# Optimization experiments

Measured on AMD Instinct MI355X. Metric: run time of the kernel, lower is better.

## Reference

```python
import jax, jax.numpy as jnp
import numpy as np


def setup_inputs() -> dict:
    key = jax.random.key(0)
    ks = jax.random.split(key, 6)
    B, S, T, E, D = 16, 128, 128, 512, 512  # batch, enc steps, dec steps, enc units, dec units
    scale = 0.05
    return {
        "enc": jax.random.normal(ks[0], (B, S, E), dtype=jnp.float32),
        "dec": jax.random.normal(ks[1], (B, T, D), dtype=jnp.float32),
        "W1": jax.random.normal(ks[2], (E, E), dtype=jnp.float32) * scale,
        "W2": jax.random.normal(ks[3], (D, E), dtype=jnp.float32) * scale,
        "b": jax.random.normal(ks[4], (1, 1, E), dtype=jnp.float32) * scale,
        "V": jax.random.normal(ks[5], (E, 1), dtype=jnp.float32) * scale,
    }


def reference(enc, dec, W1, W2, b, V):
    # Vectorized Bahdanau additive attention (the original loops over decoder
    # timesteps with keras.backend.rnn; the steps are independent so we batch them).
    W1_hs = jnp.einsum('bse,ef->bsf', enc, W1)            # [B,S,E] (computed once, not per step)
    W2_ht = jnp.einsum('btd,de->bte', dec, W2)            # [B,T,E]
    # tanh(W1.hs + W2.ht + b): broadcast to [B,T,S,E]
    scores = jnp.tanh(W1_hs[:, None, :, :] + W2_ht[:, :, None, :] + b)
    logits = jnp.einsum('btse,e->bts', scores, V[:, 0])   # [B,T,S]
    attn_weights = jax.nn.softmax(logits, axis=-1)        # softmax over encoder steps
    context_vectors = jnp.einsum('bts,bse->bte', attn_weights, enc)  # [B,T,E]
    return (context_vectors, attn_weights)
```

## Files before the change

kernel.cpp:

```cpp
#include <hip/hip_runtime.h>
#include <hip/hip_bf16.h>
#include <cstddef>


constexpr int nBt = 16, nSq = 128, nTq = 128, nEd = 512;

typedef __attribute__((ext_vector_type(4))) float f32x4;
typedef __attribute__((ext_vector_type(8))) short s16x8;

#define PRESCALE 2.8853900817779268f
#define LOG2E 1.4426950408889634f

__device__ __forceinline__ unsigned short to_bf(float f) {
    unsigned u = __builtin_bit_cast(unsigned, f);
    return (unsigned short)((u + 0x7FFFu + ((u >> 16) & 1u)) >> 16);
}
__device__ __forceinline__ float from_bf(unsigned short h) {
    unsigned u = ((unsigned)h) << 16;
    return __builtin_bit_cast(float, u);
}

__global__ __launch_bounds__(256) void kPrep(
    const float* __restrict__ W1, const float* __restrict__ W2,
    unsigned short* __restrict__ WT,
    const float* __restrict__ enc, unsigned short* __restrict__ encT)
{
    __shared__ float tl[32][33];
    const int r  = threadIdx.x >> 3;
    const int c4 = (threadIdx.x & 7) * 4;
    int bid = blockIdx.x;

    if (bid < 512) {
        const int z = bid >> 8;
        const int yx = bid & 255;
        const int kB = (yx >> 4) * 32;
        const int nB = (yx & 15) * 32;
        const float* W = z ? W2 : W1;
        const float4 v = *(const float4*)&W[(size_t)(kB + r) * nEd + nB + c4];
        tl[r][c4 + 0] = v.x; tl[r][c4 + 1] = v.y;
        tl[r][c4 + 2] = v.z; tl[r][c4 + 3] = v.w;
        __syncthreads();
        unsigned short hh[4], ll[4];
        #pragma unroll
        for (int i = 0; i < 4; ++i) {
            const float x = tl[c4 + i][r];
            hh[i] = to_bf(x);
            ll[i] = to_bf(x - from_bf(hh[i]));
        }
        const size_t o = ((size_t)z * nEd + nB + r) * nEd + kB + c4;
        *(ushort4*)&WT[o] = *(ushort4*)hh;
        *(ushort4*)&WT[(size_t)2 * nEd * nEd + o] = *(ushort4*)ll;
    } else {
        bid -= 512;
        const int b = bid >> 6;
        const int r6 = bid & 63;
        const int eB = (r6 & 15) * 32;
        const int sB = (r6 >> 4) * 32;
        const float4 v = *(const float4*)&enc[((size_t)b * nSq + sB + r) * nEd + eB + c4];
        tl[r][c4 + 0] = v.x; tl[r][c4 + 1] = v.y;
        tl[r][c4 + 2] = v.z; tl[r][c4 + 3] = v.w;
        __syncthreads();
        unsigned short o[4];
        #pragma unroll
        for (int i = 0; i < 4; ++i) o[i] = to_bf(tl[c4 + i][r]);
        *(ushort4*)&encT[((size_t)b * nEd + eB + r) * nSq + sB + c4] = *(ushort4*)o;
    }
}

__global__ __launch_bounds__(256) void kEncT(
    const float* __restrict__ enc, unsigned short* __restrict__ encT)
{
    const int b = blockIdx.z;
    __shared__ float tl[32][33];
    const int r  = threadIdx.x >> 3;
    const int c4 = (threadIdx.x & 7) * 4;
    const int sB = blockIdx.y * 32;
    const int eB = blockIdx.x * 32;
    const float4 v = *(const float4*)&enc[((size_t)b * nSq + sB + r) * nEd + eB + c4];
    tl[r][c4 + 0] = v.x; tl[r][c4 + 1] = v.y;
    tl[r][c4 + 2] = v.z; tl[r][c4 + 3] = v.w;
    __syncthreads();
    unsigned short o[4];
    #pragma unroll
    for (int i = 0; i < 4; ++i) o[i] = to_bf(tl[c4 + i][r]);
    *(ushort4*)&encT[((size_t)b * nEd + eB + r) * nSq + sB + c4] = *(ushort4*)o;
}

__global__ __launch_bounds__(256) void kMgemmB(
    const float* __restrict__ A0, const float* __restrict__ A1,
    const unsigned short* __restrict__ WT, const float* __restrict__ bias,
    float* __restrict__ C0, float* __restrict__ C1)
{
    const int z = blockIdx.z;
    const float* __restrict__ A = z ? A1 : A0;
    const unsigned short* __restrict__ Wh = WT + (size_t)z * nEd * nEd;
    const unsigned short* __restrict__ Wl = Wh + (size_t)2 * nEd * nEd;
    float* __restrict__ C = z ? C1 : C0;

    __shared__ unsigned short sAh[32][72];
    __shared__ unsigned short sAl[32][72];
    __shared__ unsigned short sBh[128][72];
    __shared__ unsigned short sBl[128][72];

    const int tid  = threadIdx.x;
    const int lane = tid & 63;
    const int wv   = tid >> 6;
    const int rowB = blockIdx.y * 32;
    const int colB = blockIdx.x * 128;

    const int ar = tid >> 3, ak = (tid & 7) * 8;
    const int br = tid >> 1, bc = (tid & 1) * 32;

    f32x4 acc[2][2] = {};
    const int l15 = lane & 15;
    const int kh  = lane >> 4;

    for (int k0 = 0; k0 < nEd; k0 += 64) {
        const float4 ga0 = *(const float4*)&A[(size_t)(rowB + ar) * nEd + k0 + ak];
        const float4 ga1 = *(const float4*)&A[(size_t)(rowB + ar) * nEd + k0 + ak + 4];
        const size_t wo = (size_t)(colB + br) * nEd + k0 + bc;
        s16x8 gh[4], gl[4];
        #pragma unroll
        for (int j = 0; j < 4; ++j) {
            gh[j] = *(const s16x8*)&Wh[wo + 8 * j];
            gl[j] = *(const s16x8*)&Wl[wo + 8 * j];
        }

        __syncthreads();
        {
            const float a8[8] = {ga0.x, ga0.y, ga0.z, ga0.w,
                                 ga1.x, ga1.y, ga1.z, ga1.w};
            unsigned short h[8], l[8];
            #pragma unroll
            for (int i = 0; i < 8; ++i) {
                h[i] = to_bf(a8[i]);
                l[i] = to_bf(a8[i] - from_bf(h[i]));
            }
            *(ushort4*)&sAh[ar][ak]     = *(ushort4*)&h[0];
            *(ushort4*)&sAh[ar][ak + 4] = *(ushort4*)&h[4];
            *(ushort4*)&sAl[ar][ak]     = *(ushort4*)&l[0];
            *(ushort4*)&sAl[ar][ak + 4] = *(ushort4*)&l[4];
        }
        #pragma unroll
        for (int j = 0; j < 4; ++j) {
            *(s16x8*)&sBh[br][bc + 8 * j] = gh[j];
            *(s16x8*)&sBl[br][bc + 8 * j] = gl[j];
        }
        __syncthreads();

        #pragma unroll
        for (int kk = 0; kk < 2; ++kk) {
            s16x8 fAh[2], fAl[2], fBh[2], fBl[2];
            #pragma unroll
            for (int mi = 0; mi < 2; ++mi) {
                fAh[mi] = *(const s16x8*)&sAh[mi * 16 + l15][kk * 32 + kh * 8];
                fAl[mi] = *(const s16x8*)&sAl[mi * 16 + l15][kk * 32 + kh * 8];
            }
            #pragma unroll
            for (int ni = 0; ni < 2; ++ni) {
                fBh[ni] = *(const s16x8*)&sBh[wv * 32 + ni * 16 + l15][kk * 32 + kh * 8];
                fBl[ni] = *(const s16x8*)&sBl[wv * 32 + ni * 16 + l15][kk * 32 + kh * 8];
            }
            #pragma unroll
            for (int mi = 0; mi < 2; ++mi)
                #pragma unroll
                for (int ni = 0; ni < 2; ++ni) {
                    f32x4 a = acc[mi][ni];
                    a = __builtin_amdgcn_mfma_f32_16x16x32_bf16(fAh[mi], fBh[ni], a, 0, 0, 0);
                    a = __builtin_amdgcn_mfma_f32_16x16x32_bf16(fAl[mi], fBh[ni], a, 0, 0, 0);
                    a = __builtin_amdgcn_mfma_f32_16x16x32_bf16(fAh[mi], fBl[ni], a, 0, 0, 0);
                    acc[mi][ni] = a;
                }
        }
    }

    #pragma unroll
    for (int ni = 0; ni < 2; ++ni) {
        const int col = colB + wv * 32 + ni * 16 + l15;
        const float bval = z ? bias[col] : 0.0f;
        #pragma unroll
        for (int mi = 0; mi < 2; ++mi) {
            #pragma unroll
            for (int r = 0; r < 4; ++r) {
                const int row = rowB + mi * 16 + kh * 4 + r;
                C[(size_t)row * nEd + col] =
                    __builtin_amdgcn_exp2f((acc[mi][ni][r] + bval) * PRESCALE);
            }
        }
    }
}

__global__ __launch_bounds__(256, 8) void kLogits(
    const float* __restrict__ X1e,
    const float* __restrict__ X2e,
    const float* __restrict__ V,
    float* __restrict__ lg)
{
    const int tg = blockIdx.x, sg = blockIdx.y, b = blockIdx.z;
    const int tid  = threadIdx.x;
    const int lane = tid & 63;
    const int w    = tid >> 6;
    const int s0 = sg * 32 + w * 8;
    const int t0 = tg * 2;

    const float4* vp = (const float4*)V;
    float4 n0 = vp[lane * 2], n1 = vp[lane * 2 + 1];
    n0.x *= -2.f; n0.y *= -2.f; n0.z *= -2.f; n0.w *= -2.f;
    n1.x *= -2.f; n1.y *= -2.f; n1.z *= -2.f; n1.w *= -2.f;

    float4 c0[2], c1[2];
    #pragma unroll
    for (int i = 0; i < 2; ++i) {
        const float4* xp = (const float4*)(X2e + ((size_t)b * nTq + t0 + i) * nEd);
        c0[i] = xp[lane * 2];
        c1[i] = xp[lane * 2 + 1];
    }

    const float* X1b = X1e + (size_t)b * nSq * nEd;
    float4 x0 = ((const float4*)(X1b + (size_t)s0 * nEd))[lane * 2];
    float4 x1 = ((const float4*)(X1b + (size_t)s0 * nEd))[lane * 2 + 1];

    #pragma unroll
    for (int si = 0; si < 8; ++si) {
        const float4 cx0 = x0, cx1 = x1;
        if (si < 7) {
            const float4* np = (const float4*)(X1b + (size_t)(s0 + si + 1) * nEd);
            x0 = np[lane * 2];
            x1 = np[lane * 2 + 1];
        }
        float a0, a1;
        a0  = n0.x * __builtin_amdgcn_rcpf(cx0.x * c0[0].x + 1.0f);
        a1  = n0.x * __builtin_amdgcn_rcpf(cx0.x * c0[1].x + 1.0f);
        a0 += n0.y * __builtin_amdgcn_rcpf(cx0.y * c0[0].y + 1.0f);
        a1 += n0.y * __builtin_amdgcn_rcpf(cx0.y * c0[1].y + 1.0f);
        a0 += n0.z * __builtin_amdgcn_rcpf(cx0.z * c0[0].z + 1.0f);
        a1 += n0.z * __builtin_amdgcn_rcpf(cx0.z * c0[1].z + 1.0f);
        a0 += n0.w * __builtin_amdgcn_rcpf(cx0.w * c0[0].w + 1.0f);
        a1 += n0.w * __builtin_amdgcn_rcpf(cx0.w * c0[1].w + 1.0f);
        a0 += n1.x * __builtin_amdgcn_rcpf(cx1.x * c1[0].x + 1.0f);
        a1 += n1.x * __builtin_amdgcn_rcpf(cx1.x * c1[1].x + 1.0f);
        a0 += n1.y * __builtin_amdgcn_rcpf(cx1.y * c1[0].y + 1.0f);
        a1 += n1.y * __builtin_amdgcn_rcpf(cx1.y * c1[1].y + 1.0f);
        a0 += n1.z * __builtin_amdgcn_rcpf(cx1.z * c1[0].z + 1.0f);
        a1 += n1.z * __builtin_amdgcn_rcpf(cx1.z * c1[1].z + 1.0f);
        a0 += n1.w * __builtin_amdgcn_rcpf(cx1.w * c1[0].w + 1.0f);
        a1 += n1.w * __builtin_amdgcn_rcpf(cx1.w * c1[1].w + 1.0f);

        const float p0 = a0 + __shfl_xor(a0, 1);
        const float p1 = a1 + __shfl_xor(a1, 1);
        float q = (lane & 1) ? p1 : p0;
        q += __shfl_xor(q, 2);
        q += __shfl_xor(q, 4);
        q += __shfl_xor(q, 8);
        q += __shfl_xor(q, 16);
        q += __shfl_xor(q, 32);
        if (lane < 2)
            lg[((size_t)b * nTq + t0 + lane) * nSq + s0 + si] = q;
    }
}

__global__ __launch_bounds__(256) void kSoftW(float* __restrict__ attnw)
{
    const int bt = blockIdx.x * 4 + (threadIdx.x >> 6);
    const int lane = threadIdx.x & 63;
    const float l0 = attnw[(size_t)bt * nSq + lane];
    const float l1 = attnw[(size_t)bt * nSq + lane + 64];
    float m = fmaxf(l0, l1);
    #pragma unroll
    for (int off = 32; off >= 1; off >>= 1)
        m = fmaxf(m, __shfl_xor(m, off));
    const float e0 = __builtin_amdgcn_exp2f((l0 - m) * LOG2E);
    const float e1 = __builtin_amdgcn_exp2f((l1 - m) * LOG2E);
    float sum = e0 + e1;
    #pragma unroll
    for (int off = 32; off >= 1; off >>= 1)
        sum += __shfl_xor(sum, off);
    const float inv = __builtin_amdgcn_rcpf(sum);
    attnw[(size_t)bt * nSq + lane]      = e0 * inv;
    attnw[(size_t)bt * nSq + lane + 64] = e1 * inv;
}

__global__ __launch_bounds__(256) void kCtxMM(
    const float* __restrict__ attnw,
    const unsigned short* __restrict__ encT,
    float* __restrict__ ctx)
{
    const int b  = blockIdx.z;
    const int tB = blockIdx.y * 32;
    const int eB = blockIdx.x * 64;

    __shared__ unsigned short sA[32][136];
    __shared__ unsigned short sB[64][136];

    const int tid  = threadIdx.x;
    const int lane = tid & 63;
    const int w    = tid >> 6;
    const int wm = (w >> 1) * 16;
    const int wn = (w & 1) * 32;
    const int l15 = lane & 15;
    const int kh  = lane >> 4;

    {
        const int r = tid >> 3, c = (tid & 7) * 16;
        const float* ap = &attnw[((size_t)b * nTq + tB + r) * nSq + c];
        unsigned short h[16];
        #pragma unroll
        for (int q = 0; q < 4; ++q) {
            const float4 v = *(const float4*)(ap + 4 * q);
            h[4 * q + 0] = to_bf(v.x); h[4 * q + 1] = to_bf(v.y);
            h[4 * q + 2] = to_bf(v.z); h[4 * q + 3] = to_bf(v.w);
        }
        *(s16x8*)&sA[r][c]     = *(s16x8*)&h[0];
        *(s16x8*)&sA[r][c + 8] = *(s16x8*)&h[8];
    }
    {
        const int r = tid >> 2, c = (tid & 3) * 32;
        const size_t o = ((size_t)b * nEd + eB + r) * nSq + c;
        *(s16x8*)&sB[r][c]      = *(const s16x8*)&encT[o];
        *(s16x8*)&sB[r][c + 8]  = *(const s16x8*)&encT[o + 8];
        *(s16x8*)&sB[r][c + 16] = *(const s16x8*)&encT[o + 16];
        *(s16x8*)&sB[r][c + 24] = *(const s16x8*)&encT[o + 24];
    }
    __syncthreads();

    f32x4 acc[2] = {};
    #pragma unroll
    for (int kk = 0; kk < 4; ++kk) {
        const s16x8 fA = *(const s16x8*)&sA[wm + l15][kk * 32 + kh * 8];
        #pragma unroll
        for (int ni = 0; ni < 2; ++ni) {
            const s16x8 fB = *(const s16x8*)&sB[wn + ni * 16 + l15][kk * 32 + kh * 8];
            acc[ni] = __builtin_amdgcn_mfma_f32_16x16x32_bf16(fA, fB, acc[ni], 0, 0, 0);
        }
    }

    #pragma unroll
    for (int ni = 0; ni < 2; ++ni) {
        const int e = eB + wn + ni * 16 + l15;
        #pragma unroll
        for (int r = 0; r < 4; ++r) {
            const int t = tB + wm + kh * 4 + r;
            ctx[((size_t)b * nTq + t) * nEd + e] = acc[ni][r];
        }
    }
}

extern "C" void kernel_launch(void* const* d_in, const int* in_sizes, int n_in,
                              void* d_out, int out_size, void* d_ws, size_t ws_size,
                              hipStream_t stream) {
    const float* enc = (const float*)d_in[0];
    const float* dec = (const float*)d_in[1];
    const float* W1  = (const float*)d_in[2];
    const float* W2  = (const float*)d_in[3];
    const float* bv  = (const float*)d_in[4];
    const float* V   = (const float*)d_in[5];

    float* ctx   = (float*)d_out;
    float* attnw = (float*)d_out + (size_t)nBt * nTq * nEd;

    unsigned short* WT = (unsigned short*)d_out;

    float* ws0 = (float*)d_ws;
    float* ws1 = ws0 + (size_t)nBt * nSq * nEd;

    const size_t eight_mb = (size_t)8 * 1024 * 1024;
    const bool early = ws_size >= eight_mb + (size_t)2 * 1024 * 1024 + 4096;
    unsigned short* encT = early
        ? (unsigned short*)((char*)d_ws + eight_mb)
        : (unsigned short*)d_ws;

    if (early) {
        kPrep<<<dim3(1536), dim3(256), 0, stream>>>(W1, W2, WT, enc, encT);
        kMgemmB<<<dim3(nEd / 128, (nBt * nSq) / 32, 2), dim3(256), 0, stream>>>(
            enc, dec, WT, bv, ws0, ws1);
        kLogits<<<dim3(nTq / 2, 4, nBt), dim3(256), 0, stream>>>(ws0, ws1, V, attnw);
    } else {
        kPrep<<<dim3(512), dim3(256), 0, stream>>>(W1, W2, WT, enc, encT);
        kMgemmB<<<dim3(nEd / 128, (nBt * nSq) / 32, 2), dim3(256), 0, stream>>>(
            enc, dec, WT, bv, ws0, ws1);
        kLogits<<<dim3(nTq / 2, 4, nBt), dim3(256), 0, stream>>>(ws0, ws1, V, attnw);
        kEncT<<<dim3(nEd / 32, nSq / 32, nBt), dim3(256), 0, stream>>>(enc, encT);
    }
    kSoftW<<<dim3((nBt * nTq) / 4), dim3(256), 0, stream>>>(attnw);
    kCtxMM<<<dim3(nEd / 64, nTq / 32, nBt), dim3(256), 0, stream>>>(
        attnw, encT, ctx);
}
```

Baseline: 52.39 us.

## Fuse softmax into logits kernel and pair reciprocals to halve rcp count

```diff
diff --git a/kernel.cpp b/kernel.cpp
--- a/kernel.cpp
+++ b/kernel.cpp
@@ -18,6 +18,17 @@
 __device__ __forceinline__ float from_bf(unsigned short h) {
     unsigned u = ((unsigned)h) << 16;
     return __builtin_bit_cast(float, u);
+}
+
+__device__ __forceinline__ void pair_acc(
+    float xa, float xb, float ca, float cb, float na, float nb, float& acc)
+{
+    const float A = fmaf(xa, ca, 1.0f);
+    const float B = fmaf(xb, cb, 1.0f);
+    const float r = __builtin_amdgcn_rcpf(A * B);
+    float num = na * B;
+    num = fmaf(nb, A, num);
+    acc = fmaf(num, r, acc);
 }
 
 __global__ __launch_bounds__(256) void kPrep(
@@ -190,18 +201,20 @@
     }
 }
 
-__global__ __launch_bounds__(256, 8) void kLogits(
+__global__ __launch_bounds__(256) void kLogSm(
     const float* __restrict__ X1e,
     const float* __restrict__ X2e,
     const float* __restrict__ V,
-    float* __restrict__ lg)
-{
-    const int tg = blockIdx.x, sg = blockIdx.y, b = blockIdx.z;
+    float* __restrict__ attnw)
+{
+    const int tg = blockIdx.x, b = blockIdx.y;
     const int tid  = threadIdx.x;
     const int lane = tid & 63;
     const int w    = tid >> 6;
-    const int s0 = sg * 32 + w * 8;
+    const int s0 = w * 32;
     const int t0 = tg * 2;
+
+    __shared__ float sm[2][nSq];
 
     const float4* vp = (const float4*)V;
     float4 n0 = vp[lane * 2], n1 = vp[lane * 2 + 1];
@@ -220,31 +233,23 @@
     float4 x0 = ((const float4*)(X1b + (size_t)s0 * nEd))[lane * 2];
     float4 x1 = ((const float4*)(X1b + (size_t)s0 * nEd))[lane * 2 + 1];
 
-    #pragma unroll
-    for (int si = 0; si < 8; ++si) {
+    #pragma unroll 4
+    for (int si = 0; si < 32; ++si) {
         const float4 cx0 = x0, cx1 = x1;
-        if (si < 7) {
+        if (si < 31) {
             const float4* np = (const float4*)(X1b + (size_t)(s0 + si + 1) * nEd);
             x0 = np[lane * 2];
             x1 = np[lane * 2 + 1];
         }
-        float a0, a1;
-        a0  = n0.x * __builtin_amdgcn_rcpf(cx0.x * c0[0].x + 1.0f);
-        a1  = n0.x * __builtin_amdgcn_rcpf(cx0.x * c0[1].x + 1.0f);
-        a0 += n0.y * __builtin_amdgcn_rcpf(cx0.y * c0[0].y + 1.0f);
-        a1 += n0.y * __builtin_amdgcn_rcpf(cx0.y * c0[1].y + 1.0f);
-        a0 += n0.z * __builtin_amdgcn_rcpf(cx0.z * c0[0].z + 1.0f);
-        a1 += n0.z * __builtin_amdgcn_rcpf(cx0.z * c0[1].z + 1.0f);
-        a0 += n0.w * __builtin_amdgcn_rcpf(cx0.w * c0[0].w + 1.0f);
-        a1 += n0.w * __builtin_amdgcn_rcpf(cx0.w * c0[1].w + 1.0f);
-        a0 += n1.x * __builtin_amdgcn_rcpf(cx1.x * c1[0].x + 1.0f);
-        a1 += n1.x * __builtin_amdgcn_rcpf(cx1.x * c1[1].x + 1.0f);
-        a0 += n1.y * __builtin_amdgcn_rcpf(cx1.y * c1[0].y + 1.0f);
-        a1 += n1.y * __builtin_amdgcn_rcpf(cx1.y * c1[1].y + 1.0f);
-        a0 += n1.z * __builtin_amdgcn_rcpf(cx1.z * c1[0].z + 1.0f);
-        a1 += n1.z * __builtin_amdgcn_rcpf(cx1.z * c1[1].z + 1.0f);
-        a0 += n1.w * __builtin_amdgcn_rcpf(cx1.w * c1[0].w + 1.0f);
-        a1 += n1.w * __builtin_amdgcn_rcpf(cx1.w * c1[1].w + 1.0f);
+        float a0 = 0.f, a1 = 0.f;
+        pair_acc(cx0.x, cx0.y, c0[0].x, c0[0].y, n0.x, n0.y, a0);
+        pair_acc(cx0.z, cx0.w, c0[0].z, c0[0].w, n0.z, n0.w, a0);
+        pair_acc(cx1.x, cx1.y, c1[0].x, c1[0].y, n1.x, n1.y, a0);
+        pair_acc(cx1.z, cx1.w, c1[0].z, c1[0].w, n1.z, n1.w, a0);
+        pair_acc(cx0.x, cx0.y, c0[1].x, c0[1].y, n0.x, n0.y, a1);
+        pair_acc(cx0.z, cx0.w, c0[1].z, c0[1].w, n0.z, n0.w, a1);
+        pair_acc(cx1.x, cx1.y, c1[1].x, c1[1].y, n1.x, n1.y, a1);
+        pair_acc(cx1.z, cx1.w, c1[1].z, c1[1].w, n1.z, n1.w, a1);
 
         const float p0 = a0 + __shfl_xor(a0, 1);
         const float p1 = a1 + __shfl_xor(a1, 1);
@@ -254,30 +259,27 @@
         q += __shfl_xor(q, 8);
         q += __shfl_xor(q, 16);
         q += __shfl_xor(q, 32);
-        if (lane < 2)
-            lg[((size_t)b * nTq + t0 + lane) * nSq + s0 + si] = q;
-    }
-}
-
-__global__ __launch_bounds__(256) void kSoftW(float* __restrict__ attnw)
-{
-    const int bt = blockIdx.x * 4 + (threadIdx.x >> 6);
-    const int lane = threadIdx.x & 63;
-    const float l0 = attnw[(size_t)bt * nSq + lane];
-    const float l1 = attnw[(size_t)bt * nSq + lane + 64];
-    float m = fmaxf(l0, l1);
-    #pragma unroll
-    for (int off = 32; off >= 1; off >>= 1)
-        m = fmaxf(m, __shfl_xor(m, off));
-    const float e0 = __builtin_amdgcn_exp2f((l0 - m) * LOG2E);
-    const float e1 = __builtin_amdgcn_exp2f((l1 - m) * LOG2E);
-    float sum = e0 + e1;
-    #pragma unroll
-    for (int off = 32; off >= 1; off >>= 1)
-        sum += __shfl_xor(sum, off);
-    const float inv = __builtin_amdgcn_rcpf(sum);
-    attnw[(size_t)bt * nSq + lane]      = e0 * inv;
-    attnw[(size_t)bt * nSq + lane + 64] = e1 * inv;
+        if (lane < 2) sm[lane][s0 + si] = q;
+    }
+    __syncthreads();
+
+    if (w < 2) {
+        const float l0 = sm[w][lane], l1 = sm[w][lane + 64];
+        float m = fmaxf(l0, l1);
+        #pragma unroll
+        for (int off = 32; off >= 1; off >>= 1)
+            m = fmaxf(m, __shfl_xor(m, off));
+        const float e0 = __builtin_amdgcn_exp2f((l0 - m) * LOG2E);
+        const float e1 = __builtin_amdgcn_exp2f((l1 - m) * LOG2E);
+        float sum = e0 + e1;
+        #pragma unroll
+        for (int off = 32; off >= 1; off >>= 1)
+            sum += __shfl_xor(sum, off);
+        const float inv = __builtin_amdgcn_rcpf(sum);
+        float* ap = attnw + ((size_t)b * nTq + t0 + w) * nSq;
+        ap[lane]      = e0 * inv;
+        ap[lane + 64] = e1 * inv;
+    }
 }
 
 __global__ __launch_bounds__(256) void kCtxMM(
@@ -373,15 +375,14 @@
         kPrep<<<dim3(1536), dim3(256), 0, stream>>>(W1, W2, WT, enc, encT);
         kMgemmB<<<dim3(nEd / 128, (nBt * nSq) / 32, 2), dim3(256), 0, stream>>>(
             enc, dec, WT, bv, ws0, ws1);
-        kLogits<<<dim3(nTq / 2, 4, nBt), dim3(256), 0, stream>>>(ws0, ws1, V, attnw);
+        kLogSm<<<dim3(nTq / 2, nBt), dim3(256), 0, stream>>>(ws0, ws1, V, attnw);
     } else {
         kPrep<<<dim3(512), dim3(256), 0, stream>>>(W1, W2, WT, enc, encT);
         kMgemmB<<<dim3(nEd / 128, (nBt * nSq) / 32, 2), dim3(256), 0, stream>>>(
             enc, dec, WT, bv, ws0, ws1);
-        kLogits<<<dim3(nTq / 2, 4, nBt), dim3(256), 0, stream>>>(ws0, ws1, V, attnw);
+        kLogSm<<<dim3(nTq / 2, nBt), dim3(256), 0, stream>>>(ws0, ws1, V, attnw);
         kEncT<<<dim3(nEd / 32, nSq / 32, nBt), dim3(256), 0, stream>>>(enc, encT);
     }
-    kSoftW<<<dim3((nBt * nTq) / 4), dim3(256), 0, stream>>>(attnw);
     kCtxMM<<<dim3(nEd / 64, nTq / 32, nBt), dim3(256), 0, stream>>>(
         attnw, encT, ctx);
 }
```

New measurement: 51.13 us. 1.02x faster.
